# Kernel tuning notes

Hardware: AMD Instinct MI355X
Metric: run time of the kernel (lower is better)

Reference implementation:

```python
import jax, jax.numpy as jnp
import numpy as np

B, N_I, N_H1, N_H2, N_H3, N_H4 = 4096, 1024, 1024, 1024, 2048, 1024


def _linear_params(key, n_out, n_in, gain=1.0):
    kw, kb = jax.random.split(key)
    # xavier_uniform on weight, torch default uniform bias ~ U(-1/sqrt(n_in), 1/sqrt(n_in))
    limit = gain * np.sqrt(6.0 / (n_in + n_out))
    W = jax.random.uniform(kw, (n_out, n_in), jnp.float32, -limit, limit)
    bl = 1.0 / np.sqrt(n_in)
    b = jax.random.uniform(kb, (n_out,), jnp.float32, -bl, bl)
    return W, b


def setup_inputs() -> dict:
    key = jax.random.key(0)
    ks = jax.random.split(key, 16)
    inp = {
        "X": jax.random.normal(ks[0], (B, N_I), jnp.float32),
        "hidden1": jax.random.normal(ks[1], (B, N_H1), jnp.float32),
        "hidden2": jax.random.normal(ks[2], (B, N_H2), jnp.float32),
        "cell1": jax.random.normal(ks[3], (B, N_H1), jnp.float32),
        "cell2": jax.random.normal(ks[4], (B, N_H2), jnp.float32),
    }
    # LSTM1 gates: Linear(n_i + n_h1, n_h1)
    inp["Wf1"], inp["bf1"] = _linear_params(ks[5], N_H1, N_I + N_H1, 1.0)
    inp["Wi1"], inp["bi1"] = _linear_params(ks[6], N_H1, N_I + N_H1, 1.0)
    inp["Wc1"], inp["bc1"] = _linear_params(ks[7], N_H1, N_I + N_H1, 5.0 / 3.0)
    inp["Wo1"], inp["bo1"] = _linear_params(ks[8], N_H1, N_I + N_H1, 1.0)
    # LSTM2 gates: Linear(n_h1 + n_h2, n_h2)
    inp["Wf2"], inp["bf2"] = _linear_params(ks[9], N_H2, N_H1 + N_H2, 1.0)
    inp["Wi2"], inp["bi2"] = _linear_params(ks[10], N_H2, N_H1 + N_H2, 1.0)
    inp["Wc2"], inp["bc2"] = _linear_params(ks[11], N_H2, N_H1 + N_H2, 5.0 / 3.0)
    inp["Wo2"], inp["bo2"] = _linear_params(ks[12], N_H2, N_H1 + N_H2, 1.0)
    # MLP head
    inp["W3"], inp["b3"] = _linear_params(ks[13], N_H3, N_H2, np.sqrt(2.0))
    inp["W4"], inp["b4"] = _linear_params(ks[14], N_H4, N_H3, 1.0)
    return inp


def _lstm_cell(x, h, c, Wf, bf, Wi, bi, Wc, bc, Wo, bo):
    z = jnp.concatenate([x, h], axis=1)           # [B, n_i + n_h]
    f = jax.nn.sigmoid(z @ Wf.T + bf)
    i = jax.nn.sigmoid(z @ Wi.T + bi)
    cand = jnp.tanh(z @ Wc.T + bc)
    o = jax.nn.sigmoid(z @ Wo.T + bo)
    h_new = o * jnp.tanh(cand)                    # NOTE: double tanh, faithful to source
    c_new = f * c + cand * i
    return h_new, c_new


def reference(X, hidden1, hidden2, cell1, cell2,
              Wf1, bf1, Wi1, bi1, Wc1, bc1, Wo1, bo1,
              Wf2, bf2, Wi2, bi2, Wc2, bc2, Wo2, bo2,
              W3, b3, W4, b4):
    h1, c1 = _lstm_cell(X, hidden1, cell1, Wf1, bf1, Wi1, bi1, Wc1, bc1, Wo1, bo1)
    h2, c2 = _lstm_cell(h1, hidden2, cell2, Wf2, bf2, Wi2, bi2, Wc2, bc2, Wo2, bo2)
    out3 = jax.nn.relu(h2 @ W3.T + b3)
    out = out3 @ W4.T + b4
    return (out, h1, h2, c1, c2)
```

## Files before the change

### kernel.cpp

```cpp
#include <hip/hip_runtime.h>
#include <hip/hip_bf16.h>
#include <stdint.h>

typedef unsigned short u16;
typedef __bf16 bf16x8 __attribute__((ext_vector_type(8)));
typedef float f32x4 __attribute__((ext_vector_type(4)));
typedef float f32x8 __attribute__((ext_vector_type(8)));

#define BM 128
#define BN 128
#define BK 64

struct SegArgs {
  const u16* W[4];
  const float* b[4];
  void* out[4];
  int act[4];
  int bf16out[4];
};

struct LstmArgs {
  const u16* W[4];
  const float* b[4];
  const float* cold;
  float* h;
  float* c;
  u16*   hb;
};

__device__ __forceinline__ float bf2f(u16 u) {
  union { unsigned int i; float f; } v; v.i = ((unsigned int)u) << 16; return v.f;
}
__device__ __forceinline__ u16 f2bf(float f) {
  union { float f; unsigned int i; } v; v.f = f;
  return (u16)((v.i + 0x7fffu + ((v.i >> 16) & 1u)) >> 16);
}
__device__ __forceinline__ uint4 cvt8(f32x8 v) {
  uint4 r;
  r.x = (unsigned)f2bf(v[0]) | ((unsigned)f2bf(v[1]) << 16);
  r.y = (unsigned)f2bf(v[2]) | ((unsigned)f2bf(v[3]) << 16);
  r.z = (unsigned)f2bf(v[4]) | ((unsigned)f2bf(v[5]) << 16);
  r.w = (unsigned)f2bf(v[6]) | ((unsigned)f2bf(v[7]) << 16);
  return r;
}
__device__ __forceinline__ float actf(float x, int act) {
  if (act == 1) return 1.0f / (1.0f + __expf(-x));
  if (act == 2) {
    float xc = fminf(fmaxf(x, -15.0f), 15.0f);
    float e = __expf(2.0f * xc);
    return (e - 1.0f) / (e + 1.0f);
  }
  if (act == 3) return fmaxf(x, 0.0f);
  return x;
}

struct CvtArgs { const float* src[10]; u16* dst[10]; };
__global__ void cvt_f2b(CvtArgs a) {
  const float* s = a.src[blockIdx.y];
  u16* d = a.dst[blockIdx.y];
  int i0 = (blockIdx.x * 256 + threadIdx.x) * 8;
  f32x8 v = *(const f32x8*)(s + i0);
  *(uint4*)(d + i0) = cvt8(v);
}

__global__ __launch_bounds__(256, 2) void gemm_lstm(
    const u16* __restrict__ A0, const u16* __restrict__ A1, int KA0, int K,
    LstmArgs La)
{
  __shared__ u16 As[BM * BK];
  __shared__ u16 Bs[BN * BK];

  const int tid  = threadIdx.x;
  const int lane = tid & 63;
  const int wave = tid >> 6;
  const int mBlock = blockIdx.x * BM;
  const int nTile  = blockIdx.y;
  const int wm = wave & 1, wn = wave >> 1;

  const u16* pA[4];
  const u16* pB[4];
#pragma unroll
  for (int it = 0; it < 4; ++it) {
    int s  = it * 256 + tid;
    int m  = s >> 3;
    int kc = (s & 7) ^ (m & 7);
    int gate = m & 3;
    int realcol = nTile * 32 + (m >> 2);
    const u16* w = (gate == 0) ? La.W[0] : (gate == 1) ? La.W[1]
                 : (gate == 2) ? La.W[2] : La.W[3];
    pB[it] = w + (size_t)realcol * (size_t)K + kc * 8;
    pA[it] = A0 + (size_t)(mBlock + m) * (size_t)KA0 + kc * 8;
  }

  const f32x4 zero = {0.f, 0.f, 0.f, 0.f};
  f32x4 acc[4][4];
#pragma unroll
  for (int i = 0; i < 4; ++i)
#pragma unroll
    for (int j = 0; j < 4; ++j) acc[i][j] = zero;

  for (int kb = 0; kb < K; kb += BK) {
    if (kb == KA0) {
#pragma unroll
      for (int it = 0; it < 4; ++it) {
        int s  = it * 256 + tid;
        int m  = s >> 3;
        int kc = (s & 7) ^ (m & 7);
        pA[it] = A1 + (size_t)(mBlock + m) * (size_t)(K - KA0) + kc * 8;
      }
    }
#pragma unroll
    for (int it = 0; it < 4; ++it) {
      u16* dA = &As[(it * 256 + wave * 64) * 8];
      u16* dB = &Bs[(it * 256 + wave * 64) * 8];
      __builtin_amdgcn_global_load_lds((void*)pA[it], (void*)dA, 16, 0, 0);
      __builtin_amdgcn_global_load_lds((void*)pB[it], (void*)dB, 16, 0, 0);
      pA[it] += BK; pB[it] += BK;
    }
    __syncthreads();

#pragma unroll
    for (int ko = 0; ko < 2; ++ko) {
      bf16x8 af[4], bfr[4];
      int kcb = ko * 4 + (lane >> 4);
      int p = kcb ^ (lane & 7);
#pragma unroll
      for (int t = 0; t < 4; ++t) {
        int ml = wm * 64 + t * 16 + (lane & 15);
        af[t]  = *(const bf16x8*)&As[(ml * 8 + p) * 8];
        int nl = wn * 64 + t * 16 + (lane & 15);
        bfr[t] = *(const bf16x8*)&Bs[(nl * 8 + p) * 8];
      }
#pragma unroll
      for (int tm = 0; tm < 4; ++tm)
#pragma unroll
        for (int tn = 0; tn < 4; ++tn)
          acc[tm][tn] = __builtin_amdgcn_mfma_f32_16x16x32_bf16(af[tm], bfr[tn], acc[tm][tn], 0, 0, 0);
    }
    __syncthreads();
  }

  const int g  = lane & 3;
  const int cl = lane & 15;
  const int q4 = (lane >> 4) * 4;
  const bool isT = (g == 2);
  const float* bsel = (g == 0) ? La.b[0] : (g == 1) ? La.b[1]
                    : (g == 2) ? La.b[2] : La.b[3];
  const bool g1 = (g & 1) != 0, g2v = (g & 2) != 0;
#pragma unroll
  for (int tn = 0; tn < 4; ++tn) {
    int col = nTile * 32 + wn * 16 + tn * 4 + (cl >> 2);
    float bv = bsel[col];
#pragma unroll
    for (int tm = 0; tm < 4; ++tm) {
      int rowbase = mBlock + wm * 64 + tm * 16 + q4;
#pragma unroll
      for (int r = 0; r < 4; ++r) {
        float x  = acc[tm][tn][r] + bv;
        float xc = isT ? fminf(fmaxf(x, -15.f), 15.f) : x;
        float e  = __expf(isT ? 2.f * xc : -x);
        float a  = isT ? (e - 1.f) / (e + 1.f) : 1.f / (1.f + e);
        float x1 = __shfl_xor(a, 1);
        float x2 = __shfl_xor(a, 2);
        float x3 = __shfl_xor(a, 3);
        float fv = g1 ? (g2v ? x3 : x1) : (g2v ? x2 : a);
        float iv = g1 ? (g2v ? x2 : a ) : (g2v ? x3 : x1);
        float cd = g1 ? (g2v ? x1 : x3) : (g2v ? a  : x2);
        float ov = g1 ? (g2v ? a  : x2) : (g2v ? x1 : x3);
        if (g == r) {
          size_t idx = (size_t)(rowbase + r) * 1024 + col;
          float cn = fv * La.cold[idx] + cd * iv;
          float e2 = __expf(2.f * cd);
          float th = (e2 - 1.f) / (e2 + 1.f);
          float hv = ov * th;
          La.h[idx]  = hv;
          La.c[idx]  = cn;
          La.hb[idx] = f2bf(hv);
        }
      }
    }
  }
}

__global__ __launch_bounds__(256, 2) void gemm_bt(
    const u16* __restrict__ A0, const u16* __restrict__ A1, int KA0, int K,
    SegArgs segs, int tileShift, int ldOut)
{
  __shared__ u16 As[BM * BK];
  __shared__ u16 Bs[BN * BK];

  const int tid  = threadIdx.x;
  const int lane = tid & 63;
  const int wave = tid >> 6;
  const int mBlock = blockIdx.x * BM;
  const int seg   = blockIdx.y >> tileShift;
  const int nTile = blockIdx.y & ((1 << tileShift) - 1);

  const u16* Wp = segs.W[seg];
  const int wm = wave & 1, wn = wave >> 1;

  const f32x4 zero = {0.f, 0.f, 0.f, 0.f};
  f32x4 acc[4][4];
#pragma unroll
  for (int i = 0; i < 4; ++i)
#pragma unroll
    for (int j = 0; j < 4; ++j) acc[i][j] = zero;

  for (int kb = 0; kb < K; kb += BK) {
    const u16* Aseg; int ka; int ldA;
    if (kb < KA0) { Aseg = A0; ka = kb;       ldA = KA0; }
    else          { Aseg = A1; ka = kb - KA0; ldA = K - KA0; }

#pragma unroll
    for (int it = 0; it < 4; ++it) {
      int s = it * 256 + tid;
      int m = s >> 3;
      int p = s & 7;
      int kc = p ^ (m & 7);
      const u16* srcA = Aseg + (size_t)(mBlock + m) * (size_t)ldA + (ka + kc * 8);
      const u16* srcB = Wp + (size_t)(nTile * BN + m) * (size_t)K + (kb + kc * 8);
      u16* dA = &As[(it * 256 + wave * 64) * 8];
      u16* dB = &Bs[(it * 256 + wave * 64) * 8];
      __builtin_amdgcn_global_load_lds((void*)srcA, (void*)dA, 16, 0, 0);
      __builtin_amdgcn_global_load_lds((void*)srcB, (void*)dB, 16, 0, 0);
    }
    __syncthreads();

#pragma unroll
    for (int ko = 0; ko < 2; ++ko) {
      bf16x8 af[4], bfr[4];
      int kcb = ko * 4 + (lane >> 4);
      int p = kcb ^ (lane & 7);
#pragma unroll
      for (int t = 0; t < 4; ++t) {
        int ml = wm * 64 + t * 16 + (lane & 15);
        af[t]  = *(const bf16x8*)&As[(ml * 8 + p) * 8];
        int nl = wn * 64 + t * 16 + (lane & 15);
        bfr[t] = *(const bf16x8*)&Bs[(nl * 8 + p) * 8];
      }
#pragma unroll
      for (int tm = 0; tm < 4; ++tm)
#pragma unroll
        for (int tn = 0; tn < 4; ++tn)
          acc[tm][tn] = __builtin_amdgcn_mfma_f32_16x16x32_bf16(af[tm], bfr[tn], acc[tm][tn], 0, 0, 0);
    }
    __syncthreads();
  }

  const float* bp = segs.b[seg];
  const int act = segs.act[seg];
  const int isBf = segs.bf16out[seg];
  u16*   opb = (u16*)segs.out[seg];
  float* opf = (float*)segs.out[seg];
  const int q  = lane >> 4;
  const int cl = lane & 15;
#pragma unroll
  for (int tn = 0; tn < 4; ++tn) {
    int col = nTile * BN + wn * 64 + tn * 16 + cl;
    float bv = bp[col];
#pragma unroll
    for (int tm = 0; tm < 4; ++tm) {
      int row = mBlock + wm * 64 + tm * 16 + q * 4;
#pragma unroll
      for (int r = 0; r < 4; ++r) {
        float v = actf(acc[tm][tn][r] + bv, act);
        size_t idx = (size_t)(row + r) * (size_t)ldOut + col;
        if (isBf) opb[idx] = f2bf(v); else opf[idx] = v;
      }
    }
  }
}

extern "C" void kernel_launch(void* const* d_in, const int* in_sizes, int n_in,
                              void* d_out, int out_size, void* d_ws, size_t ws_size,
                              hipStream_t stream)
{
  const size_t P   = 4096ull * 1024ull;
  const size_t C2M = 2097152ull;

  const float* X   = (const float*)d_in[0];
  const float* h1i = (const float*)d_in[1];
  const float* h2i = (const float*)d_in[2];
  const float* c1i = (const float*)d_in[3];
  const float* c2i = (const float*)d_in[4];
  const float* Wf1 = (const float*)d_in[5];  const float* bf1_ = (const float*)d_in[6];
  const float* Wi1 = (const float*)d_in[7];  const float* bi1_ = (const float*)d_in[8];
  const float* Wc1 = (const float*)d_in[9];  const float* bc1_ = (const float*)d_in[10];
  const float* Wo1 = (const float*)d_in[11]; const float* bo1_ = (const float*)d_in[12];
  const float* Wf2 = (const float*)d_in[13]; const float* bf2_ = (const float*)d_in[14];
  const float* Wi2 = (const float*)d_in[15]; const float* bi2_ = (const float*)d_in[16];
  const float* Wc2 = (const float*)d_in[17]; const float* bc2_ = (const float*)d_in[18];
  const float* Wo2 = (const float*)d_in[19]; const float* bo2_ = (const float*)d_in[20];
  const float* W3  = (const float*)d_in[21]; const float* b3_  = (const float*)d_in[22];
  const float* W4  = (const float*)d_in[23]; const float* b4_  = (const float*)d_in[24];

  float* out = (float*)d_out;
  float* h1  = out + P;
  float* h2  = out + 2 * P;
  float* c1  = out + 3 * P;
  float* c2  = out + 4 * P;

  char* ws = (char*)d_ws;
  u16* Areg  = (u16*)(ws + (32ull << 20));
  u16* Breg  = (u16*)(ws + (48ull << 20));
  u16* Creg  = (u16*)(ws + (56ull << 20));
  u16* Ereg  = (u16*)(ws + (64ull << 20));
  u16* Freg  = (u16*)(ws + (72ull << 20));

  dim3 blk(256, 1, 1);

  CvtArgs ca;
  ca.src[0]=Wf1;        ca.dst[0]=Areg;
  ca.src[1]=Wi1;        ca.dst[1]=Areg + C2M;
  ca.src[2]=Wc1;        ca.dst[2]=Areg + 2*C2M;
  ca.src[3]=Wo1;        ca.dst[3]=Areg + 3*C2M;
  ca.src[4]=X;          ca.dst[4]=Breg;
  ca.src[5]=X + C2M;    ca.dst[5]=Breg + C2M;
  ca.src[6]=h1i;        ca.dst[6]=Creg;
  ca.src[7]=h1i + C2M;  ca.dst[7]=Creg + C2M;
  ca.src[8]=W3;         ca.dst[8]=Freg;
  ca.src[9]=W4;         ca.dst[9]=Freg + C2M;
  cvt_f2b<<<dim3(1024, 10, 1), blk, 0, stream>>>(ca);

  LstmArgs l1;
  l1.W[0]=Areg; l1.W[1]=Areg+C2M; l1.W[2]=Areg+2*C2M; l1.W[3]=Areg+3*C2M;
  l1.b[0]=bf1_; l1.b[1]=bi1_; l1.b[2]=bc1_; l1.b[3]=bo1_;
  l1.cold=c1i; l1.h=h1; l1.c=c1; l1.hb=Ereg;
  gemm_lstm<<<dim3(32,32,1), blk, 0, stream>>>(Breg, Creg, 1024, 2048, l1);

  CvtArgs cb;
  cb.src[0]=Wf2;        cb.dst[0]=Areg;
  cb.src[1]=Wi2;        cb.dst[1]=Areg + C2M;
  cb.src[2]=Wc2;        cb.dst[2]=Areg + 2*C2M;
  cb.src[3]=Wo2;        cb.dst[3]=Areg + 3*C2M;
  cb.src[4]=h2i;        cb.dst[4]=Breg;
  cb.src[5]=h2i + C2M;  cb.dst[5]=Breg + C2M;
  cvt_f2b<<<dim3(1024, 6, 1), blk, 0, stream>>>(cb);

  LstmArgs l2;
  l2.W[0]=Areg; l2.W[1]=Areg+C2M; l2.W[2]=Areg+2*C2M; l2.W[3]=Areg+3*C2M;
  l2.b[0]=bf2_; l2.b[1]=bi2_; l2.b[2]=bc2_; l2.b[3]=bo2_;
  l2.cold=c2i; l2.h=h2; l2.c=c2; l2.hb=Creg;
  gemm_lstm<<<dim3(32,32,1), blk, 0, stream>>>(Ereg, Breg, 1024, 2048, l2);

  SegArgs s3;
  for (int g = 0; g < 4; ++g) { s3.W[g]=Freg; s3.b[g]=b3_; s3.out[g]=Areg; s3.act[g]=3; s3.bf16out[g]=1; }
  gemm_bt<<<dim3(32,16,1), blk, 0, stream>>>(Creg, (const u16*)nullptr, 1024, 1024, s3, 4, 2048);

  SegArgs s4;
  for (int g = 0; g < 4; ++g) { s4.W[g]=Freg+C2M; s4.b[g]=b4_; s4.out[g]=out; s4.act[g]=0; s4.bf16out[g]=0; }
  gemm_bt<<<dim3(32,8,1), blk, 0, stream>>>(Areg, (const u16*)nullptr, 2048, 2048, s4, 3, 1024);
}
```

Before: 538.6 us.

## Group LSTM gate columns per block and stage gate activations through LDS

The weight tile is now laid out so each group of 32 columns belongs to one gate instead of interleaving gates per column. The epilogue applies each gate's activation, writes the result as bf16 into shared memory, and after a barrier each thread combines the four gates for 16 contiguous columns. This replaces the per-element shuffles and scattered single-element stores with vectorised loads of the old cell state and vectorised stores of h, c and bf16 h. In exchange it adds a shared-memory round trip and a barrier, and rounds the gate values to bf16 before the cell update, which costs some accuracy.

```diff
diff --git a/kernel.cpp b/kernel.cpp
--- a/kernel.cpp
+++ b/kernel.cpp
@@ -63,33 +63,30 @@
   *(uint4*)(d + i0) = cvt8(v);
 }
 
-__global__ __launch_bounds__(256, 2) void gemm_lstm(
+__global__ __launch_bounds__(256, 2) void gemm_lstm2(
     const u16* __restrict__ A0, const u16* __restrict__ A1, int KA0, int K,
     LstmArgs La)
 {
-  __shared__ u16 As[BM * BK];
-  __shared__ u16 Bs[BN * BK];
+  __shared__ u16 smem[2 * 8192];
+  u16* As = smem;
+  u16* Bs = smem + 8192;
 
   const int tid  = threadIdx.x;
   const int lane = tid & 63;
   const int wave = tid >> 6;
   const int mBlock = blockIdx.x * BM;
   const int nTile  = blockIdx.y;
+  const int colBase32 = nTile * 32;
   const int wm = wave & 1, wn = wave >> 1;
 
+  const int rsub = tid >> 3;
+  const int kc   = (tid & 7) ^ (rsub & 7);
   const u16* pA[4];
   const u16* pB[4];
 #pragma unroll
   for (int it = 0; it < 4; ++it) {
-    int s  = it * 256 + tid;
-    int m  = s >> 3;
-    int kc = (s & 7) ^ (m & 7);
-    int gate = m & 3;
-    int realcol = nTile * 32 + (m >> 2);
-    const u16* w = (gate == 0) ? La.W[0] : (gate == 1) ? La.W[1]
-                 : (gate == 2) ? La.W[2] : La.W[3];
-    pB[it] = w + (size_t)realcol * (size_t)K + kc * 8;
-    pA[it] = A0 + (size_t)(mBlock + m) * (size_t)KA0 + kc * 8;
+    pB[it] = La.W[it] + (size_t)(colBase32 + rsub) * (size_t)K + kc * 8;
+    pA[it] = A0 + (size_t)(mBlock + it * 32 + rsub) * (size_t)KA0 + kc * 8;
   }
 
   const f32x4 zero = {0.f, 0.f, 0.f, 0.f};
@@ -102,12 +99,8 @@
   for (int kb = 0; kb < K; kb += BK) {
     if (kb == KA0) {
 #pragma unroll
-      for (int it = 0; it < 4; ++it) {
-        int s  = it * 256 + tid;
-        int m  = s >> 3;
-        int kc = (s & 7) ^ (m & 7);
-        pA[it] = A1 + (size_t)(mBlock + m) * (size_t)(K - KA0) + kc * 8;
-      }
+      for (int it = 0; it < 4; ++it)
+        pA[it] = A1 + (size_t)(mBlock + it * 32 + rsub) * (size_t)(K - KA0) + kc * 8;
     }
 #pragma unroll
     for (int it = 0; it < 4; ++it) {
@@ -140,45 +133,84 @@
     __syncthreads();
   }
 
-  const int g  = lane & 3;
   const int cl = lane & 15;
   const int q4 = (lane >> 4) * 4;
-  const bool isT = (g == 2);
-  const float* bsel = (g == 0) ? La.b[0] : (g == 1) ? La.b[1]
-                    : (g == 2) ? La.b[2] : La.b[3];
-  const bool g1 = (g & 1) != 0, g2v = (g & 2) != 0;
 #pragma unroll
   for (int tn = 0; tn < 4; ++tn) {
-    int col = nTile * 32 + wn * 16 + tn * 4 + (cl >> 2);
-    float bv = bsel[col];
+    const int g = wn * 2 + (tn >> 1);
+    const float* bg = (tn >> 1) ? (wn ? La.b[3] : La.b[1])
+                                : (wn ? La.b[2] : La.b[0]);
+    const bool isT = (wn == 1) && ((tn >> 1) == 0);
+    const int col = (tn & 1) * 16 + cl;
+    float bv = bg[colBase32 + col];
 #pragma unroll
     for (int tm = 0; tm < 4; ++tm) {
-      int rowbase = mBlock + wm * 64 + tm * 16 + q4;
+      const int rbase = wm * 64 + tm * 16 + q4;
 #pragma unroll
       for (int r = 0; r < 4; ++r) {
-        float x  = acc[tm][tn][r] + bv;
-        float xc = isT ? fminf(fmaxf(x, -15.f), 15.f) : x;
-        float e  = __expf(isT ? 2.f * xc : -x);
-        float a  = isT ? (e - 1.f) / (e + 1.f) : 1.f / (1.f + e);
-        float x1 = __shfl_xor(a, 1);
-        float x2 = __shfl_xor(a, 2);
-        float x3 = __shfl_xor(a, 3);
-        float fv = g1 ? (g2v ? x3 : x1) : (g2v ? x2 : a);
-        float iv = g1 ? (g2v ? x2 : a ) : (g2v ? x3 : x1);
-        float cd = g1 ? (g2v ? x1 : x3) : (g2v ? a  : x2);
-        float ov = g1 ? (g2v ? a  : x2) : (g2v ? x1 : x3);
-        if (g == r) {
-          size_t idx = (size_t)(rowbase + r) * 1024 + col;
-          float cn = fv * La.cold[idx] + cd * iv;
-          float e2 = __expf(2.f * cd);
-          float th = (e2 - 1.f) / (e2 + 1.f);
-          float hv = ov * th;
-          La.h[idx]  = hv;
-          La.c[idx]  = cn;
-          La.hb[idx] = f2bf(hv);
+        float x = acc[tm][tn][r] + bv;
+        float a;
+        if (isT) {
+          float xc = fminf(fmaxf(x, -15.f), 15.f);
+          float e = __expf(2.f * xc);
+          a = (e - 1.f) / (e + 1.f);
+        } else {
+          a = 1.f / (1.f + __expf(-x));
         }
-      }
-    }
+        int row = rbase + r;
+        smem[g * 4096 + row * 32 + (((col >> 3) ^ ((row >> 2) & 3)) << 3) + (col & 7)] = f2bf(a);
+      }
+    }
+  }
+  __syncthreads();
+
+  {
+    const int rowL = tid >> 1;
+    const int hf   = tid & 1;
+    const int xr   = (rowL >> 2) & 3;
+    union GU { uint4 v; u16 u[8]; };
+    GU gu[4][2];
+#pragma unroll
+    for (int g = 0; g < 4; ++g)
+#pragma unroll
+      for (int jj = 0; jj < 2; ++jj) {
+        int ch = (hf * 2 + jj) ^ xr;
+        gu[g][jj].v = *(const uint4*)&smem[g * 4096 + rowL * 32 + ch * 8];
+      }
+    size_t base = (size_t)(mBlock + rowL) * 1024 + colBase32 + hf * 16;
+    f32x8 cA = *(const f32x8*)(La.cold + base);
+    f32x8 cB = *(const f32x8*)(La.cold + base + 8);
+    f32x8 H0, H1, C0, C1;
+#pragma unroll
+    for (int j = 0; j < 8; ++j) {
+      float f  = bf2f(gu[0][0].u[j]);
+      float iv = bf2f(gu[1][0].u[j]);
+      float cd = bf2f(gu[2][0].u[j]);
+      float o  = bf2f(gu[3][0].u[j]);
+      float cn = f * cA[j] + cd * iv;
+      float e  = __expf(2.0f * cd);
+      float th = (e - 1.0f) / (e + 1.0f);
+      H0[j] = o * th;
+      C0[j] = cn;
+    }
+#pragma unroll
+    for (int j = 0; j < 8; ++j) {
+      float f  = bf2f(gu[0][1].u[j]);
+      float iv = bf2f(gu[1][1].u[j]);
+      float cd = bf2f(gu[2][1].u[j]);
+      float o  = bf2f(gu[3][1].u[j]);
+      float cn = f * cB[j] + cd * iv;
+      float e  = __expf(2.0f * cd);
+      float th = (e - 1.0f) / (e + 1.0f);
+      H1[j] = o * th;
+      C1[j] = cn;
+    }
+    *(f32x8*)(La.h + base)     = H0;
+    *(f32x8*)(La.h + base + 8) = H1;
+    *(f32x8*)(La.c + base)     = C0;
+    *(f32x8*)(La.c + base + 8) = C1;
+    *(uint4*)(La.hb + base)     = cvt8(H0);
+    *(uint4*)(La.hb + base + 8) = cvt8(H1);
   }
 }
 
@@ -326,7 +358,7 @@
   l1.W[0]=Areg; l1.W[1]=Areg+C2M; l1.W[2]=Areg+2*C2M; l1.W[3]=Areg+3*C2M;
   l1.b[0]=bf1_; l1.b[1]=bi1_; l1.b[2]=bc1_; l1.b[3]=bo1_;
   l1.cold=c1i; l1.h=h1; l1.c=c1; l1.hb=Ereg;
-  gemm_lstm<<<dim3(32,32,1), blk, 0, stream>>>(Breg, Creg, 1024, 2048, l1);
+  gemm_lstm2<<<dim3(32,32,1), blk, 0, stream>>>(Breg, Creg, 1024, 2048, l1);
 
   CvtArgs cb;
   cb.src[0]=Wf2;        cb.dst[0]=Areg;
@@ -341,7 +373,7 @@
   l2.W[0]=Areg; l2.W[1]=Areg+C2M; l2.W[2]=Areg+2*C2M; l2.W[3]=Areg+3*C2M;
   l2.b[0]=bf2_; l2.b[1]=bi2_; l2.b[2]=bc2_; l2.b[3]=bo2_;
   l2.cold=c2i; l2.h=h2; l2.c=c2; l2.hb=Creg;
-  gemm_lstm<<<dim3(32,32,1), blk, 0, stream>>>(Ereg, Breg, 1024, 2048, l2);
+  gemm_lstm2<<<dim3(32,32,1), blk, 0, stream>>>(Ereg, Breg, 1024, 2048, l2);
 
   SegArgs s3;
   for (int g = 0; g < 4; ++g) { s3.W[g]=Freg; s3.b[g]=b3_; s3.out[g]=Areg; s3.act[g]=3; s3.bf16out[g]=1; }
```

Measured after the change: 468.8 us. -13.0%, faster.
